# Performance work log

Hardware: AMD Instinct MI355X
Metric: run time of the kernel (lower is better)

## Reference

```python
import jax, jax.numpy as jnp
import numpy as np

TEMP1, TEMP2, TEMP3 = 4.0, 5.0, 10.0  # forward() default temps
EPS = 1e-8


def setup_inputs() -> dict:
    key = jax.random.key(0)
    k1, k2 = jax.random.split(key)
    B, L, D = 64, 64, 512
    return {
        "ecg_embs": jax.random.normal(k1, (B, L, D), dtype=jnp.float32),
        "sent_embs": jax.random.normal(k2, (B, L, D), dtype=jnp.float32),
    }


def reference(ecg_embs, sent_embs):
    # Fully-batched version of the original per-sample Python loop.
    # i indexes the sentence (query) sample, j the ecg (context) sample.
    B, L, D = ecg_embs.shape
    # scores[i,j,s,q] = <ecg[j,s,:], sent[i,q,:]>  == contextT @ query in torch
    scores = jnp.einsum('jsd,iqd->ijsq', ecg_embs, sent_embs)
    # 1st softmax over query axis q
    attn = jax.nn.softmax(scores, axis=-1)
    # transpose to (i,j,q,s), temperature-scale, 2nd softmax over source axis s
    attn = jax.nn.softmax(TEMP1 * jnp.swapaxes(attn, -1, -2), axis=-1)  # (i,j,q,s)
    # weightedContext[i,j,q,:] = sum_s attn[i,j,q,s] * ecg[j,s,:]
    wctx = jnp.einsum('ijqs,jsd->ijqd', attn, ecg_embs)
    sent = sent_embs[:, None]  # (i,1,q,d) broadcast over j
    w12 = jnp.sum(sent * wctx, axis=-1)
    w1 = jnp.linalg.norm(sent, axis=-1)
    w2 = jnp.linalg.norm(wctx, axis=-1)
    cos = w12 / jnp.maximum(w1 * w2, EPS)  # (i,j,q)
    # row_sim.mul_(temp2).exp_().sum(dim=1).log() ; similarities[j,i] (cat along dim=1)
    sim = TEMP3 * jnp.log(jnp.sum(jnp.exp(TEMP2 * cos), axis=-1)).T  # (j,i)
    labels = jnp.arange(B)
    logp0 = jax.nn.log_softmax(sim, axis=-1)
    logp1 = jax.nn.log_softmax(sim.T, axis=-1)
    loss0 = -jnp.mean(logp0[labels, labels])
    loss1 = -jnp.mean(logp1[labels, labels])
    # att_maps: list of attn[i] from iteration i == diagonal (i==j) attention,
    # each shaped (1, queryL, ih=1, iw=sourceL); stacked -> (B, 1, L, 1, L)
    att_maps = attn[labels, labels][:, None, :, None, :]
    return (loss0 + loss1) / 2.0, att_maps
```

## Files before the change

kernel.cpp:

```cpp
#include <hip/hip_runtime.h>
#include <math.h>

typedef __attribute__((ext_vector_type(8))) short short8;
typedef __attribute__((ext_vector_type(4))) float f32x4;
typedef unsigned int uint;
typedef unsigned short ushort;

#define T1 4.0f
#define T2 5.0f
#define T3 10.0f
#define EPSF 1e-8f

__device__ inline ushort f2bf(float x) {
    union { float f; uint u; } a; a.f = x;
    uint r = a.u + 0x7FFFu + ((a.u >> 16) & 1u);
    return (ushort)(r >> 16);
}
__device__ inline float bf2f(ushort h) {
    union { uint u; float f; } a; a.u = ((uint)h) << 16;
    return a.f;
}

#define GLDS(gsrc, ldst) \
    __builtin_amdgcn_global_load_lds( \
        (const __attribute__((address_space(1))) uint*)(gsrc), \
        (__attribute__((address_space(3))) uint*)(ldst), 16, 0, 0)

__global__ __launch_bounds__(256) void prep_kernel(
        const float* __restrict__ ecg, const float* __restrict__ sent,
        char* __restrict__ EH, char* __restrict__ EL,
        char* __restrict__ SH, char* __restrict__ SL, float* __restrict__ w1) {
    __shared__ float partial[256];
    const int bid = blockIdx.x;
    const int tensor = bid >> 6, idx = bid & 63;
    const float* src = (tensor ? sent : ecg) + (size_t)idx * 32768;
    char* dh = (tensor ? SH : EH) + (size_t)idx * 65536;
    char* dl = (tensor ? SL : EL) + (size_t)idx * 65536;
    const int tid = threadIdx.x;
    const int r = tid & 63;
    float s2 = 0.f;
    #pragma unroll
    for (int it = 0; it < 4; it++) {
        int kc = it * 4 + (tid >> 6);
        const float* p = src + r * 512 + kc * 32;
        char* oh = dh + kc * 4096 + r * 64;
        char* ol = dl + kc * 4096 + r * 64;
        #pragma unroll
        for (int c = 0; c < 4; c++) {
            float4 v0 = *(const float4*)(p + c * 8);
            float4 v1 = *(const float4*)(p + c * 8 + 4);
            float x[8] = {v0.x, v0.y, v0.z, v0.w, v1.x, v1.y, v1.z, v1.w};
            uint hw[4], lw[4];
            #pragma unroll
            for (int e = 0; e < 4; e++) {
                float a0 = x[2 * e], a1 = x[2 * e + 1];
                ushort h0 = f2bf(a0), h1 = f2bf(a1);
                hw[e] = (uint)h0 | ((uint)h1 << 16);
                ushort l0 = f2bf(a0 - bf2f(h0)), l1 = f2bf(a1 - bf2f(h1));
                lw[e] = (uint)l0 | ((uint)l1 << 16);
                s2 += a0 * a0 + a1 * a1;
            }
            int phys = (c + (r >> 1)) & 3;
            uint4 H; H.x = hw[0]; H.y = hw[1]; H.z = hw[2]; H.w = hw[3];
            *(uint4*)(oh + phys * 16) = H;
            uint4 L; L.x = lw[0]; L.y = lw[1]; L.z = lw[2]; L.w = lw[3];
            *(uint4*)(ol + phys * 16) = L;
        }
    }
    partial[tid] = s2;
    __syncthreads();
    if (tensor == 1 && tid < 64) {
        float t = partial[tid] + partial[tid + 64] + partial[tid + 128] + partial[tid + 192];
        w1[idx * 64 + tid] = sqrtf(t);
    }
}

__global__ __launch_bounds__(256) void gprep_kernel(const float* __restrict__ ecg,
        char* __restrict__ Gp) {
    __shared__ __align__(16) float Et[64 * 36];
    const int j = blockIdx.x;
    const float* E = ecg + (size_t)j * (64 * 512);
    const int tid = threadIdx.x;
    const int ty = tid >> 4, tx = tid & 15;
    const int sr = tid >> 3, sc = tid & 7;
    float acc[4][4];
    #pragma unroll
    for (int a = 0; a < 4; a++)
        #pragma unroll
        for (int b = 0; b < 4; b++) acc[a][b] = 0.f;

    for (int k0 = 0; k0 < 512; k0 += 32) {
        float4 e0 = *(const float4*)(E + (size_t)sr * 512 + k0 + sc * 4);
        float4 e1 = *(const float4*)(E + (size_t)(sr + 32) * 512 + k0 + sc * 4);
        __syncthreads();
        *(float4*)(Et + sr * 36 + sc * 4)        = e0;
        *(float4*)(Et + (sr + 32) * 36 + sc * 4) = e1;
        __syncthreads();
        #pragma unroll
        for (int kk = 0; kk < 8; kk++) {
            float4 ea[4], eb[4];
            #pragma unroll
            for (int a = 0; a < 4; a++) ea[a] = *(const float4*)(Et + (a * 16 + ty) * 36 + kk * 4);
            #pragma unroll
            for (int b = 0; b < 4; b++) eb[b] = *(const float4*)(Et + (b * 16 + tx) * 36 + kk * 4);
            #pragma unroll
            for (int a = 0; a < 4; a++)
                #pragma unroll
                for (int b = 0; b < 4; b++)
                    acc[a][b] += ea[a].x * eb[b].x + ea[a].y * eb[b].y +
                                 ea[a].z * eb[b].z + ea[a].w * eb[b].w;
        }
    }
    #pragma unroll
    for (int a = 0; a < 4; a++)
        #pragma unroll
        for (int b = 0; b < 4; b++) {
            float g = acc[a][b];
            ushort h = f2bf(g);
            ushort l = f2bf(g - bf2f(h));
            int t = a * 16 + ty, u = b * 16 + tx;
            int phys = ((u >> 3) + t) & 7;
            char* base = Gp + (size_t)j * 16384 + t * 128 + phys * 16 + (u & 7) * 2;
            *(ushort*)base = h;
            *(ushort*)(base + 8192) = l;
        }
}

__global__ __launch_bounds__(256, 4) void pair_kernel(
        const char* __restrict__ EH, const char* __restrict__ EL,
        const char* __restrict__ SH, const char* __restrict__ SL,
        const char* __restrict__ Gp, const float* __restrict__ w1g,
        float* __restrict__ simval, float* __restrict__ out) {

    __shared__ __align__(16) char lds[33792];
    __shared__ float mz[64], w12a[64], w2sq[64];

    const int tid = threadIdx.x;
    const int bn = blockIdx.x;
    const int xcd = bn & 7, slot = bn >> 3;
    const int T = xcd * 8 + (slot >> 4);
    const int wp = slot & 15;
    const int bi = (T >> 3) * 4 + (wp >> 2);
    const int bj = (T & 7) * 4 + (wp & 3);
    const int i0 = bi * 2, j0 = bj * 2;

    const int wv = tid >> 6, lane = tid & 63;
    const int wq = wv >> 1, wn = wv & 1;
    const int quad = lane >> 4, ln = lane & 15;

    int aoff[4], boff[4];
    #pragma unroll
    for (int mi = 0; mi < 4; mi++) {
        int R = 64 * (mi >> 1) + 32 * wq + 16 * (mi & 1) + ln;
        aoff[mi] = R * 64 + ((quad + (R >> 1)) & 3) * 16;
    }
    #pragma unroll
    for (int ni = 0; ni < 4; ni++) {
        int R = 64 * (ni >> 1) + 32 * wn + 16 * (ni & 1) + ln;
        boff[ni] = 16384 + R * 64 + ((quad + (R >> 1)) & 3) * 16;
    }

    const char* gA; const char* gB; int ldoff;
    if (wv == 0)      { gA = EH + (size_t)j0 * 65536;       gB = EH + (size_t)(j0 + 1) * 65536; ldoff = 0; }
    else if (wv == 1) { gA = EL + (size_t)j0 * 65536;       gB = EL + (size_t)(j0 + 1) * 65536; ldoff = 8192; }
    else if (wv == 2) { gA = SH + (size_t)i0 * 65536;       gB = SH + (size_t)(i0 + 1) * 65536; ldoff = 16384; }
    else              { gA = SL + (size_t)i0 * 65536;       gB = SL + (size_t)(i0 + 1) * 65536; ldoff = 24576; }
    gA += lane * 16; gB += lane * 16;

    f32x4 acc[4][4];
    #pragma unroll
    for (int a = 0; a < 4; a++)
        #pragma unroll
        for (int b = 0; b < 4; b++) acc[a][b] = (f32x4){0.f, 0.f, 0.f, 0.f};

    for (int kc = 0; kc < 16; kc++) {
        #pragma unroll
        for (int n = 0; n < 4; n++) GLDS(gA + n * 1024, lds + ldoff + n * 1024);
        #pragma unroll
        for (int n = 0; n < 4; n++) GLDS(gB + n * 1024, lds + ldoff + 4096 + n * 1024);
        gA += 4096; gB += 4096;
        __syncthreads();
        short8 bh[4], bl[4];
        #pragma unroll
        for (int ni = 0; ni < 4; ni++) {
            bh[ni] = *(const short8*)(lds + boff[ni]);
            bl[ni] = *(const short8*)(lds + boff[ni] + 8192);
        }
        #pragma unroll
        for (int mi = 0; mi < 4; mi++) {
            short8 ah = *(const short8*)(lds + aoff[mi]);
            short8 al = *(const short8*)(lds + aoff[mi] + 8192);
            #pragma unroll
            for (int ni = 0; ni < 4; ni++) {
                acc[mi][ni] = __builtin_amdgcn_mfma_f32_16x16x32_bf16(ah, bh[ni], acc[mi][ni], 0, 0, 0);
                acc[mi][ni] = __builtin_amdgcn_mfma_f32_16x16x32_bf16(ah, bl[ni], acc[mi][ni], 0, 0, 0);
                acc[mi][ni] = __builtin_amdgcn_mfma_f32_16x16x32_bf16(al, bh[ni], acc[mi][ni], 0, 0, 0);
            }
        }
        __syncthreads();
    }

    float* Ssc = (float*)lds;
    float* yb  = (float*)lds;
    char*  Pb  = lds + 17408;

    #pragma unroll
    for (int pr = 0; pr < 4; pr++) {
        const int a = pr >> 1, b = pr & 1;
        const int i = i0 + b, j = j0 + a;

        #pragma unroll
        for (int dm = 0; dm < 2; dm++)
            #pragma unroll
            for (int dn = 0; dn < 2; dn++) {
                int s = 32 * wq + 16 * dm + quad * 4;
                int q = 32 * wn + 16 * dn + ln;
                f32x4 v = acc[2 * a + dm][2 * b + dn];
                Ssc[(s + 0) * 65 + q] = v[0];
                Ssc[(s + 1) * 65 + q] = v[1];
                Ssc[(s + 2) * 65 + q] = v[2];
                Ssc[(s + 3) * 65 + q] = v[3];
            }
        __syncthreads();

        {
            const int s = tid >> 2, c = tid & 3;
            float vv[16]; float m = -1e30f;
            #pragma unroll
            for (int t = 0; t < 16; t++) { vv[t] = Ssc[s * 65 + c * 16 + t]; m = fmaxf(m, vv[t]); }
            m = fmaxf(m, __shfl_xor(m, 1));
            m = fmaxf(m, __shfl_xor(m, 2));
            float sum = 0.f;
            #pragma unroll
            for (int t = 0; t < 16; t++) sum += __expf(vv[t] - m);
            sum += __shfl_xor(sum, 1);
            sum += __shfl_xor(sum, 2);
            if (c == 0) mz[s] = m + __logf(sum);
        }
        __syncthreads();

        {
            const int q = tid >> 2, c = tid & 3;
            float at[16];
            #pragma unroll
            for (int t = 0; t < 16; t++)
                at[t] = __expf(Ssc[(c * 16 + t) * 65 + q] - mz[c * 16 + t]);
            float m2 = -1e30f;
            #pragma unroll
            for (int t = 0; t < 16; t++) m2 = fmaxf(m2, T1 * at[t]);
            m2 = fmaxf(m2, __shfl_xor(m2, 1));
            m2 = fmaxf(m2, __shfl_xor(m2, 2));
            float sum = 0.f;
            #pragma unroll
            for (int t = 0; t < 16; t++) { at[t] = __expf(T1 * at[t] - m2); sum += at[t]; }
            sum += __shfl_xor(sum, 1);
            sum += __shfl_xor(sum, 2);
            float inv = 1.f / sum;
            #pragma unroll
            for (int t = 0; t < 16; t++) at[t] *= inv;

            float p12 = 0.f;
            #pragma unroll
            for (int t = 0; t < 16; t++) p12 += at[t] * Ssc[(c * 16 + t) * 65 + q];
            p12 += __shfl_xor(p12, 1);
            p12 += __shfl_xor(p12, 2);
            if (c == 0) w12a[q] = p12;

            if (i == j) {
                float* om = out + 1 + (size_t)i * 4096;
                #pragma unroll
                for (int t = 0; t < 16; t++) om[q * 64 + c * 16 + t] = at[t];
            }

            uint hw[8], lw[8];
            #pragma unroll
            for (int e = 0; e < 8; e++) {
                ushort h0 = f2bf(at[2 * e]), h1 = f2bf(at[2 * e + 1]);
                hw[e] = (uint)h0 | ((uint)h1 << 16);
                ushort l0 = f2bf(at[2 * e] - bf2f(h0)), l1 = f2bf(at[2 * e + 1] - bf2f(h1));
                lw[e] = (uint)l0 | ((uint)l1 << 16);
            }
            int p0 = (2 * c + q) & 7, p1 = (2 * c + 1 + q) & 7;
            uint4 W;
            W.x = hw[0]; W.y = hw[1]; W.z = hw[2]; W.w = hw[3];
            *(uint4*)(Pb + q * 128 + p0 * 16) = W;
            W.x = hw[4]; W.y = hw[5]; W.z = hw[6]; W.w = hw[7];
            *(uint4*)(Pb + q * 128 + p1 * 16) = W;
            W.x = lw[0]; W.y = lw[1]; W.z = lw[2]; W.w = lw[3];
            *(uint4*)(Pb + 8192 + q * 128 + p0 * 16) = W;
            W.x = lw[4]; W.y = lw[5]; W.z = lw[6]; W.w = lw[7];
            *(uint4*)(Pb + 8192 + q * 128 + p1 * 16) = W;
        }
        __syncthreads();

        {
            const char* gs = Gp + (size_t)j * 16384 + tid * 64;
            char* gd = lds + tid * 64;
            uint4 g0 = *(const uint4*)(gs);
            uint4 g1 = *(const uint4*)(gs + 16);
            uint4 g2 = *(const uint4*)(gs + 32);
            uint4 g3 = *(const uint4*)(gs + 48);
            *(uint4*)(gd)      = g0;
            *(uint4*)(gd + 16) = g1;
            *(uint4*)(gd + 32) = g2;
            *(uint4*)(gd + 48) = g3;
        }
        __syncthreads();

        f32x4 acc2[2][2];
        #pragma unroll
        for (int x = 0; x < 2; x++)
            #pragma unroll
            for (int y = 0; y < 2; y++) acc2[x][y] = (f32x4){0.f, 0.f, 0.f, 0.f};
        #pragma unroll
        for (int ch = 0; ch < 2; ch++) {
            short8 pah[2], pal[2], gbh[2], gbl[2];
            #pragma unroll
            for (int m2i = 0; m2i < 2; m2i++) {
                int q = 32 * wq + 16 * m2i + ln;
                int ph = ((ch * 4 + quad) + q) & 7;
                pah[m2i] = *(const short8*)(Pb + q * 128 + ph * 16);
                pal[m2i] = *(const short8*)(Pb + 8192 + q * 128 + ph * 16);
            }
            #pragma unroll
            for (int n2i = 0; n2i < 2; n2i++) {
                int u = 32 * wn + 16 * n2i + ln;
                int ph = ((ch * 4 + quad) + u) & 7;
                gbh[n2i] = *(const short8*)(lds + u * 128 + ph * 16);
                gbl[n2i] = *(const short8*)(lds + 8192 + u * 128 + ph * 16);
            }
            #pragma unroll
            for (int m2i = 0; m2i < 2; m2i++)
                #pragma unroll
                for (int n2i = 0; n2i < 2; n2i++) {
                    acc2[m2i][n2i] = __builtin_amdgcn_mfma_f32_16x16x32_bf16(pah[m2i], gbh[n2i], acc2[m2i][n2i], 0, 0, 0);
                    acc2[m2i][n2i] = __builtin_amdgcn_mfma_f32_16x16x32_bf16(pah[m2i], gbl[n2i], acc2[m2i][n2i], 0, 0, 0);
                    acc2[m2i][n2i] = __builtin_amdgcn_mfma_f32_16x16x32_bf16(pal[m2i], gbh[n2i], acc2[m2i][n2i], 0, 0, 0);
                }
        }
        __syncthreads();

        #pragma unroll
        for (int m2i = 0; m2i < 2; m2i++)
            #pragma unroll
            for (int n2i = 0; n2i < 2; n2i++) {
                int q = 32 * wq + 16 * m2i + quad * 4;
                int u = 32 * wn + 16 * n2i + ln;
                f32x4 v = acc2[m2i][n2i];
                yb[(q + 0) * 68 + u] = v[0];
                yb[(q + 1) * 68 + u] = v[1];
                yb[(q + 2) * 68 + u] = v[2];
                yb[(q + 3) * 68 + u] = v[3];
            }
        __syncthreads();

        {
            const int q = tid >> 2, c = tid & 3;
            const float* yr = yb + q * 68 + 16 * c;
            float4 y0 = *(const float4*)(yr);
            float4 y1 = *(const float4*)(yr + 4);
            float4 y2 = *(const float4*)(yr + 8);
            float4 y3 = *(const float4*)(yr + 12);
            float yv[16] = {y0.x,y0.y,y0.z,y0.w, y1.x,y1.y,y1.z,y1.w,
                            y2.x,y2.y,y2.z,y2.w, y3.x,y3.y,y3.z,y3.w};
            int p0 = (2 * c + q) & 7, p1 = (2 * c + 1 + q) & 7;
            uint4 H0 = *(const uint4*)(Pb + q * 128 + p0 * 16);
            uint4 H1 = *(const uint4*)(Pb + q * 128 + p1 * 16);
            uint4 L0 = *(const uint4*)(Pb + 8192 + q * 128 + p0 * 16);
            uint4 L1 = *(const uint4*)(Pb + 8192 + q * 128 + p1 * 16);
            uint hw[8] = {H0.x,H0.y,H0.z,H0.w, H1.x,H1.y,H1.z,H1.w};
            uint lw[8] = {L0.x,L0.y,L0.z,L0.w, L1.x,L1.y,L1.z,L1.w};
            float s = 0.f;
            #pragma unroll
            for (int e = 0; e < 8; e++) {
                float q0 = bf2f((ushort)(hw[e] & 0xFFFFu)) + bf2f((ushort)(lw[e] & 0xFFFFu));
                float q1 = bf2f((ushort)(hw[e] >> 16))     + bf2f((ushort)(lw[e] >> 16));
                s += q0 * yv[2 * e] + q1 * yv[2 * e + 1];
            }
            s += __shfl_xor(s, 1);
            s += __shfl_xor(s, 2);
            if (c == 0) w2sq[q] = s;
        }
        __syncthreads();

        if (tid < 64) {
            float w2 = sqrtf(fmaxf(w2sq[tid], 0.f));
            float cosv = w12a[tid] / fmaxf(w1g[i * 64 + tid] * w2, EPSF);
            float e = __expf(T2 * cosv);
            #pragma unroll
            for (int off = 32; off; off >>= 1) e += __shfl_down(e, off);
            if (tid == 0) simval[i * 64 + j] = T3 * __logf(e);
        }
        __syncthreads();
    }
}

__global__ void loss_kernel(const float* __restrict__ val, float* __restrict__ out) {
    int i = threadIdx.x;
    float rmax = -1e30f, cmax = -1e30f;
    for (int jj = 0; jj < 64; jj++) {
        rmax = fmaxf(rmax, val[i * 64 + jj]);
        cmax = fmaxf(cmax, val[jj * 64 + i]);
    }
    float rs = 0.f, cs = 0.f;
    for (int jj = 0; jj < 64; jj++) {
        rs += __expf(val[i * 64 + jj] - rmax);
        cs += __expf(val[jj * 64 + i] - cmax);
    }
    float rlse = rmax + __logf(rs);
    float clse = cmax + __logf(cs);
    float part = 2.f * val[i * 64 + i] - rlse - clse;
    #pragma unroll
    for (int off = 32; off; off >>= 1) part += __shfl_down(part, off);
    if (i == 0) out[0] = -part / 128.f;
}

extern "C" void kernel_launch(void* const* d_in, const int* in_sizes, int n_in,
                              void* d_out, int out_size, void* d_ws, size_t ws_size,
                              hipStream_t stream) {
    (void)in_sizes; (void)n_in; (void)out_size; (void)ws_size;
    const float* ecg  = (const float*)d_in[0];
    const float* sent = (const float*)d_in[1];
    float* out = (float*)d_out;

    char* ws = (char*)d_ws;
    float* w1v  = (float*)ws;
    float* simv = (float*)(ws + 16384);
    char* EH = ws + 32768;
    char* EL = EH + (size_t)64 * 65536;
    char* SH = EL + (size_t)64 * 65536;
    char* SL = SH + (size_t)64 * 65536;
    char* Gp = SL + (size_t)64 * 65536;

    prep_kernel <<<128, 256, 0, stream>>>(ecg, sent, EH, EL, SH, SL, w1v);
    gprep_kernel<<<64,  256, 0, stream>>>(ecg, Gp);
    pair_kernel <<<1024, 256, 0, stream>>>(EH, EL, SH, SL, Gp, w1v, simv, out);
    loss_kernel <<<1,   64,  0, stream>>>(simv, out);
}
```

Before: 169.0 us.

## Use MFMA for Gram prep, transpose score staging, batch cosine epilogue

The per-sample Gram matrix E·Eᵀ is now computed with split-bf16 MFMA from the already prepared hi/lo bf16 buffers instead of scalar FP32 FMA. The pair kernel stores MFMA accumulators transposed with vector stores and reads them back as vectors. It also defers the cosine/logsumexp epilogue for all four pairs to the end, one pair per wave, which removes per-pair barriers. The loss kernel stages the similarity matrix in LDS with 256 threads. In exchange, gprep now depends on prep_kernel's output, and Gram precision drops to the split-bf16 scheme.

```diff
diff --git a/kernel.cpp b/kernel.cpp
--- a/kernel.cpp
+++ b/kernel.cpp
@@ -10,6 +10,7 @@
 #define T2 5.0f
 #define T3 10.0f
 #define EPSF 1e-8f
+#define SST 68
 
 __device__ inline ushort f2bf(float x) {
     union { float f; uint u; } a; a.f = x;
@@ -75,55 +76,75 @@
     }
 }
 
-__global__ __launch_bounds__(256) void gprep_kernel(const float* __restrict__ ecg,
-        char* __restrict__ Gp) {
-    __shared__ __align__(16) float Et[64 * 36];
+__global__ __launch_bounds__(256) void gprep_kernel(
+        const char* __restrict__ EH, const char* __restrict__ EL, char* __restrict__ Gp) {
+    __shared__ __align__(16) char lds[8192];
     const int j = blockIdx.x;
-    const float* E = ecg + (size_t)j * (64 * 512);
     const int tid = threadIdx.x;
-    const int ty = tid >> 4, tx = tid & 15;
-    const int sr = tid >> 3, sc = tid & 7;
-    float acc[4][4];
-    #pragma unroll
-    for (int a = 0; a < 4; a++)
-        #pragma unroll
-        for (int b = 0; b < 4; b++) acc[a][b] = 0.f;
-
-    for (int k0 = 0; k0 < 512; k0 += 32) {
-        float4 e0 = *(const float4*)(E + (size_t)sr * 512 + k0 + sc * 4);
-        float4 e1 = *(const float4*)(E + (size_t)(sr + 32) * 512 + k0 + sc * 4);
-        __syncthreads();
-        *(float4*)(Et + sr * 36 + sc * 4)        = e0;
-        *(float4*)(Et + (sr + 32) * 36 + sc * 4) = e1;
-        __syncthreads();
-        #pragma unroll
-        for (int kk = 0; kk < 8; kk++) {
-            float4 ea[4], eb[4];
-            #pragma unroll
-            for (int a = 0; a < 4; a++) ea[a] = *(const float4*)(Et + (a * 16 + ty) * 36 + kk * 4);
-            #pragma unroll
-            for (int b = 0; b < 4; b++) eb[b] = *(const float4*)(Et + (b * 16 + tx) * 36 + kk * 4);
-            #pragma unroll
-            for (int a = 0; a < 4; a++)
-                #pragma unroll
-                for (int b = 0; b < 4; b++)
-                    acc[a][b] += ea[a].x * eb[b].x + ea[a].y * eb[b].y +
-                                 ea[a].z * eb[b].z + ea[a].w * eb[b].w;
-        }
-    }
-    #pragma unroll
-    for (int a = 0; a < 4; a++)
-        #pragma unroll
-        for (int b = 0; b < 4; b++) {
-            float g = acc[a][b];
-            ushort h = f2bf(g);
-            ushort l = f2bf(g - bf2f(h));
-            int t = a * 16 + ty, u = b * 16 + tx;
-            int phys = ((u >> 3) + t) & 7;
-            char* base = Gp + (size_t)j * 16384 + t * 128 + phys * 16 + (u & 7) * 2;
-            *(ushort*)base = h;
-            *(ushort*)(base + 8192) = l;
-        }
+    const int wv = tid >> 6, lane = tid & 63;
+    const int wq = wv >> 1, wn = wv & 1;
+    const int quad = lane >> 4, ln = lane & 15;
+    const char* srcH = EH + (size_t)j * 65536 + wv * 1024 + lane * 16;
+    const char* srcL = EL + (size_t)j * 65536 + wv * 1024 + lane * 16;
+
+    int ao[2], bo[2];
+    #pragma unroll
+    for (int mi = 0; mi < 2; mi++) {
+        int R = 32 * wq + 16 * mi + ln;
+        ao[mi] = R * 64 + ((quad + (R >> 1)) & 3) * 16;
+    }
+    #pragma unroll
+    for (int ni = 0; ni < 2; ni++) {
+        int R = 32 * wn + 16 * ni + ln;
+        bo[ni] = R * 64 + ((quad + (R >> 1)) & 3) * 16;
+    }
+
+    f32x4 acc[2][2];
+    #pragma unroll
+    for (int a = 0; a < 2; a++)
+        #pragma unroll
+        for (int b = 0; b < 2; b++) acc[a][b] = (f32x4){0.f, 0.f, 0.f, 0.f};
+
+    for (int kc = 0; kc < 16; kc++) {
+        GLDS(srcH + (size_t)kc * 4096, lds + wv * 1024);
+        GLDS(srcL + (size_t)kc * 4096, lds + 4096 + wv * 1024);
+        __syncthreads();
+        short8 ah[2], al[2], bh[2], bl[2];
+        #pragma unroll
+        for (int mi = 0; mi < 2; mi++) {
+            ah[mi] = *(const short8*)(lds + ao[mi]);
+            al[mi] = *(const short8*)(lds + 4096 + ao[mi]);
+        }
+        #pragma unroll
+        for (int ni = 0; ni < 2; ni++) {
+            bh[ni] = *(const short8*)(lds + bo[ni]);
+            bl[ni] = *(const short8*)(lds + 4096 + bo[ni]);
+        }
+        #pragma unroll
+        for (int mi = 0; mi < 2; mi++)
+            #pragma unroll
+            for (int ni = 0; ni < 2; ni++) {
+                acc[mi][ni] = __builtin_amdgcn_mfma_f32_16x16x32_bf16(ah[mi], bh[ni], acc[mi][ni], 0, 0, 0);
+                acc[mi][ni] = __builtin_amdgcn_mfma_f32_16x16x32_bf16(ah[mi], bl[ni], acc[mi][ni], 0, 0, 0);
+                acc[mi][ni] = __builtin_amdgcn_mfma_f32_16x16x32_bf16(al[mi], bh[ni], acc[mi][ni], 0, 0, 0);
+            }
+        __syncthreads();
+    }
+    #pragma unroll
+    for (int mi = 0; mi < 2; mi++)
+        #pragma unroll
+        for (int ni = 0; ni < 2; ni++)
+            #pragma unroll
+            for (int r = 0; r < 4; r++) {
+                int t = 32 * wq + 16 * mi + quad * 4 + r;
+                int u = 32 * wn + 16 * ni + ln;
+                float g = acc[mi][ni][r];
+                ushort h = f2bf(g);
+                ushort l = f2bf(g - bf2f(h));
+                char* base = Gp + (size_t)j * 16384 + t * 128 + (((u >> 3) + t) & 7) * 16 + (u & 7) * 2;
+                *(ushort*)base = h;
+                *(ushort*)(base + 8192) = l;
+            }
 }
 
 __global__ __launch_bounds__(256, 4) void pair_kernel(
@@ -133,7 +154,8 @@
         float* __restrict__ simval, float* __restrict__ out) {
 
     __shared__ __align__(16) char lds[33792];
-    __shared__ float mz[64], w12a[64], w2sq[64];
+    __shared__ __align__(16) float mz[64];
+    __shared__ float w12all[256], w2all[256];
 
     const int tid = threadIdx.x;
     const int bn = blockIdx.x;
@@ -200,8 +222,8 @@
         __syncthreads();
     }
 
-    float* Ssc = (float*)lds;
-    float* yb  = (float*)lds;
+    float* SsT = (float*)lds;
+    float* yT  = (float*)lds;
     char*  Pb  = lds + 17408;
 
     #pragma unroll
@@ -213,13 +235,9 @@
         for (int dm = 0; dm < 2; dm++)
             #pragma unroll
             for (int dn = 0; dn < 2; dn++) {
-                int s = 32 * wq + 16 * dm + quad * 4;
-                int q = 32 * wn + 16 * dn + ln;
-                f32x4 v = acc[2 * a + dm][2 * b + dn];
-                Ssc[(s + 0) * 65 + q] = v[0];
-                Ssc[(s + 1) * 65 + q] = v[1];
-                Ssc[(s + 2) * 65 + q] = v[2];
-                Ssc[(s + 3) * 65 + q] = v[3];
+                int s0 = 32 * wq + 16 * dm + quad * 4;
+                int q  = 32 * wn + 16 * dn + ln;
+                *(f32x4*)(SsT + q * SST + s0) = acc[2 * a + dm][2 * b + dn];
             }
         __syncthreads();
 
@@ -227,7 +245,7 @@
             const int s = tid >> 2, c = tid & 3;
             float vv[16]; float m = -1e30f;
             #pragma unroll
-            for (int t = 0; t < 16; t++) { vv[t] = Ssc[s * 65 + c * 16 + t]; m = fmaxf(m, vv[t]); }
+            for (int t = 0; t < 16; t++) { vv[t] = SsT[(16 * c + t) * SST + s]; m = fmaxf(m, vv[t]); }
             m = fmaxf(m, __shfl_xor(m, 1));
             m = fmaxf(m, __shfl_xor(m, 2));
             float sum = 0.f;
@@ -241,13 +259,20 @@
 
         {
             const int q = tid >> 2, c = tid & 3;
-            float at[16];
-            #pragma unroll
-            for (int t = 0; t < 16; t++)
-                at[t] = __expf(Ssc[(c * 16 + t) * 65 + q] - mz[c * 16 + t]);
+            float sc[16], at[16];
+            #pragma unroll
+            for (int r4 = 0; r4 < 4; r4++)
+                *(f32x4*)(sc + 4 * r4) = *(const f32x4*)(SsT + q * SST + 16 * c + 4 * r4);
+            float mzv[16];
+            #pragma unroll
+            for (int r4 = 0; r4 < 4; r4++)
+                *(f32x4*)(mzv + 4 * r4) = *(const f32x4*)(mz + 16 * c + 4 * r4);
             float m2 = -1e30f;
             #pragma unroll
-            for (int t = 0; t < 16; t++) m2 = fmaxf(m2, T1 * at[t]);
+            for (int t = 0; t < 16; t++) {
+                at[t] = __expf(sc[t] - mzv[t]);
+                m2 = fmaxf(m2, T1 * at[t]);
+            }
             m2 = fmaxf(m2, __shfl_xor(m2, 1));
             m2 = fmaxf(m2, __shfl_xor(m2, 2));
             float sum = 0.f;
@@ -256,15 +281,12 @@
             sum += __shfl_xor(sum, 1);
             sum += __shfl_xor(sum, 2);
             float inv = 1.f / sum;
-            #pragma unroll
-            for (int t = 0; t < 16; t++) at[t] *= inv;
-
             float p12 = 0.f;
             #pragma unroll
-            for (int t = 0; t < 16; t++) p12 += at[t] * Ssc[(c * 16 + t) * 65 + q];
+            for (int t = 0; t < 16; t++) { at[t] *= inv; p12 += at[t] * sc[t]; }
             p12 += __shfl_xor(p12, 1);
             p12 += __shfl_xor(p12, 2);
-            if (c == 0) w12a[q] = p12;
+            if (c == 0) w12all[pr * 64 + q] = p12;
 
             if (i == j) {
                 float* om = out + 1 + (size_t)i * 4096;
@@ -344,25 +366,14 @@
         for (int m2i = 0; m2i < 2; m2i++)
             #pragma unroll
             for (int n2i = 0; n2i < 2; n2i++) {
-                int q = 32 * wq + 16 * m2i + quad * 4;
-                int u = 32 * wn + 16 * n2i + ln;
-                f32x4 v = acc2[m2i][n2i];
-                yb[(q + 0) * 68 + u] = v[0];
-                yb[(q + 1) * 68 + u] = v[1];
-                yb[(q + 2) * 68 + u] = v[2];
-                yb[(q + 3) * 68 + u] = v[3];
+                int q0 = 32 * wq + 16 * m2i + quad * 4;
+                int t  = 32 * wn + 16 * n2i + ln;
+                *(f32x4*)(yT + t * SST + q0) = acc2[m2i][n2i];
             }
         __syncthreads();
 
         {
             const int q = tid >> 2, c = tid & 3;
-            const float* yr = yb + q * 68 + 16 * c;
-            float4 y0 = *(const float4*)(yr);
-            float4 y1 = *(const float4*)(yr + 4);
-            float4 y2 = *(const float4*)(yr + 8);
-            float4 y3 = *(const float4*)(yr + 12);
-            float yv[16] = {y0.x,y0.y,y0.z,y0.w, y1.x,y1.y,y1.z,y1.w,
-                            y2.x,y2.y,y2.z,y2.w, y3.x,y3.y,y3.z,y3.w};
             int p0 = (2 * c + q) & 7, p1 = (2 * c + 1 + q) & 7;
             uint4 H0 = *(const uint4*)(Pb + q * 128 + p0 * 16);
             uint4 H1 = *(const uint4*)(Pb + q * 128 + p1 * 16);
@@ -373,46 +384,57 @@
             float s = 0.f;
             #pragma unroll
             for (int e = 0; e < 8; e++) {
-                float q0 = bf2f((ushort)(hw[e] & 0xFFFFu)) + bf2f((ushort)(lw[e] & 0xFFFFu));
-                float q1 = bf2f((ushort)(hw[e] >> 16))     + bf2f((ushort)(lw[e] >> 16));
-                s += q0 * yv[2 * e] + q1 * yv[2 * e + 1];
+                float q0v = bf2f((ushort)(hw[e] & 0xFFFFu)) + bf2f((ushort)(lw[e] & 0xFFFFu));
+                float q1v = bf2f((ushort)(hw[e] >> 16))     + bf2f((ushort)(lw[e] >> 16));
+                s += q0v * yT[(16 * c + 2 * e) * SST + q];
+                s += q1v * yT[(16 * c + 2 * e + 1) * SST + q];
             }
             s += __shfl_xor(s, 1);
             s += __shfl_xor(s, 2);
-            if (c == 0) w2sq[q] = s;
-        }
-        __syncthreads();
-
-        if (tid < 64) {
-            float w2 = sqrtf(fmaxf(w2sq[tid], 0.f));
-            float cosv = w12a[tid] / fmaxf(w1g[i * 64 + tid] * w2, EPSF);
-            float e = __expf(T2 * cosv);
-            #pragma unroll
-            for (int off = 32; off; off >>= 1) e += __shfl_down(e, off);
-            if (tid == 0) simval[i * 64 + j] = T3 * __logf(e);
-        }
-        __syncthreads();
-    }
-}
-
-__global__ void loss_kernel(const float* __restrict__ val, float* __restrict__ out) {
-    int i = threadIdx.x;
-    float rmax = -1e30f, cmax = -1e30f;
-    for (int jj = 0; jj < 64; jj++) {
-        rmax = fmaxf(rmax, val[i * 64 + jj]);
-        cmax = fmaxf(cmax, val[jj * 64 + i]);
-    }
-    float rs = 0.f, cs = 0.f;
-    for (int jj = 0; jj < 64; jj++) {
-        rs += __expf(val[i * 64 + jj] - rmax);
-        cs += __expf(val[jj * 64 + i] - cmax);
-    }
-    float rlse = rmax + __logf(rs);
-    float clse = cmax + __logf(cs);
-    float part = 2.f * val[i * 64 + i] - rlse - clse;
-    #pragma unroll
-    for (int off = 32; off; off >>= 1) part += __shfl_down(part, off);
-    if (i == 0) out[0] = -part / 128.f;
+            if (c == 0) w2all[pr * 64 + q] = s;
+        }
+        __syncthreads();
+    }
+
+    {
+        const int pr = wv;
+        const int ii = i0 + (pr & 1), jj = j0 + (pr >> 1);
+        float w2 = sqrtf(fmaxf(w2all[pr * 64 + lane], 0.f));
+        float cosv = w12all[pr * 64 + lane] / fmaxf(w1g[ii * 64 + lane] * w2, EPSF);
+        float e = __expf(T2 * cosv);
+        #pragma unroll
+        for (int off = 32; off; off >>= 1) e += __shfl_down(e, off);
+        if (lane == 0) simval[ii * 64 + jj] = T3 * __logf(e);
+    }
+}
+
+__global__ __launch_bounds__(256) void loss_kernel(const float* __restrict__ val,
+                                                   float* __restrict__ out) {
+    __shared__ float v[4096];
+    const int tid = threadIdx.x;
+    #pragma unroll
+    for (int k = 0; k < 4; k++)
+        ((float4*)v)[tid + k * 256] = ((const float4*)val)[tid + k * 256];
+    __syncthreads();
+    if (tid < 64) {
+        int i = tid;
+        float rmax = -1e30f, cmax = -1e30f;
+        for (int jj = 0; jj < 64; jj++) {
+            rmax = fmaxf(rmax, v[i * 64 + jj]);
+            cmax = fmaxf(cmax, v[jj * 64 + i]);
+        }
+        float rs = 0.f, cs = 0.f;
+        for (int jj = 0; jj < 64; jj++) {
+            rs += __expf(v[i * 64 + jj] - rmax);
+            cs += __expf(v[jj * 64 + i] - cmax);
+        }
+        float rlse = rmax + __logf(rs);
+        float clse = cmax + __logf(cs);
+        float part = 2.f * v[i * 64 + i] - rlse - clse;
+        #pragma unroll
+        for (int off = 32; off; off >>= 1) part += __shfl_down(part, off);
+        if (i == 0) out[0] = -part / 128.f;
+    }
 }
 
 extern "C" void kernel_launch(void* const* d_in, const int* in_sizes, int n_in,
@@ -433,7 +455,7 @@
     char* Gp = SL + (size_t)64 * 65536;
 
     prep_kernel <<<128, 256, 0, stream>>>(ecg, sent, EH, EL, SH, SL, w1v);
-    gprep_kernel<<<64,  256, 0, stream>>>(ecg, Gp);
+    gprep_kernel<<<64,  256, 0, stream>>>(EH, EL, Gp);
     pair_kernel <<<1024, 256, 0, stream>>>(EH, EL, SH, SL, Gp, w1v, simv, out);
-    loss_kernel <<<1,   64,  0, stream>>>(simv, out);
-}
+    loss_kernel <<<1,   256, 0, stream>>>(simv, out);
+}
```

After: 151.3 us. 1.12x faster.
